# Optimization experiments

Hardware: AMD Instinct MI355X
Metric: run time of the kernel (lower is better)

## Reference

```python
import jax, jax.numpy as jnp
import numpy as np


def _pick(key, nodes, mask, cnt):
    # Uniformly pick one of the `cnt` entries of `nodes` where mask is True.
    r = jax.random.randint(key, (), 0, jnp.maximum(cnt, 1))
    cs = jnp.cumsum(mask.astype(jnp.int32))
    return nodes[jnp.argmax(cs == r + 1)]


def _one_walk(key, nbrs, f0, n_faces, L):
    # nbrs: [N,3] int32 neighbor table, f0: scalar start face.
    seq = jnp.zeros((L + 1,), jnp.int32).at[0].set(f0)
    visited = jnp.zeros((n_faces + 1,), bool).at[n_faces].set(True).at[f0].set(True)

    def cond(st):
        return st[2] <= L

    def body(st):
        seq, visited, i, bs, k = st
        k, k1, k2, k3 = jax.random.split(k, 4)
        cur = seq[i - 1]
        nb = nbrs[cur]                     # [3] neighbor candidates
        unv = ~visited[nb]
        cnt = unv.sum()
        need = cnt == 0                    # stuck -> backtrack
        cand = _pick(k1, nb, unv, cnt)

        def bcond(c):
            bs_c, found = c[0], c[1]
            return need & (~found) & (i > bs_c)

        def bbody(c):
            bs_c, found, ta, kk = c
            kk, kp = jax.random.split(kk)
            back = seq[i - bs_c - 1]
            bn = nbrs[back]
            bm = ~visited[bn]
            bc = bm.sum()
            f2 = bc > 0
            ta2 = _pick(kp, bn, bm, bc)
            return (jnp.where(f2, bs_c, bs_c + 2), f2, jnp.where(f2, ta2, ta), kk)

        bs_f, found, ta_bt, _ = jax.lax.while_loop(
            bcond, bbody, (bs, jnp.array(False), jnp.int32(0), k2))
        rand_node = jax.random.randint(k3, (), 0, n_faces, dtype=jnp.int32)
        to_add = jnp.where(~need, cand, jnp.where(found, ta_bt, rand_node))
        hit = need & found                 # successful backtrack
        bs_new = jnp.where(hit, bs_f, jnp.int32(1))
        i_new = jnp.where(hit, i - bs_f, i)
        ar = jnp.arange(L + 1, dtype=jnp.int32)
        # torch: replace seq[i-bs:i] with to_add on successful backtrack
        seq = jnp.where(hit & (ar >= i_new) & (ar < i), to_add, seq)
        visited = visited.at[to_add].set(True)
        seq = seq.at[i_new].set(to_add)
        return (seq, visited, i_new + 1, bs_new, k)

    seq, *_ = jax.lax.while_loop(
        cond, body, (seq, visited, jnp.int32(1), jnp.int32(1), key))
    return seq


def patch_random_walk(key, neighbors, centers, n_faces, seq_len):
    B, G = centers.shape
    keys = jax.random.split(key, B * G).reshape(B, G)
    walk_g = jax.vmap(_one_walk, in_axes=(0, None, 0, None, None))
    walk_bg = jax.vmap(walk_g, in_axes=(0, 0, 0, None, None))
    return walk_bg(keys, neighbors, centers, n_faces, seq_len)  # [B,G,L+1] int32


def setup_inputs() -> dict:
    key = jax.random.key(0)
    k1, k2, k3 = jax.random.split(key, 3)
    B, N, G = 4, 20000, 1024
    xyz = jax.random.normal(k1, (B, N, 3), dtype=jnp.float32)
    neighbors = jax.random.randint(k2, (B, N, 3), 0, N, dtype=jnp.int32)
    centers = jax.random.randint(k3, (B, G), 0, N, dtype=jnp.int32)
    return {"xyz": xyz, "neighbors": neighbors, "centers": centers,
            "n_faces": N, "seq_len": 63}


def reference(xyz, neighbors, centers, n_faces, seq_len):
    # patch_random_walk -> idx [B,G,K]; then Group.forward gather + recenter.
    idx = patch_random_walk(jax.random.key(42), neighbors, centers, n_faces, seq_len)
    gather = jax.vmap(lambda p, i: p[i])(xyz, idx)            # [B,G,K,3]
    center_xyz = jax.vmap(lambda p, c: p[c])(xyz, centers)    # [B,G,3]
    return gather - center_xyz[:, :, None, :]
```

## Files before the change

### kernel.cpp

```cpp
#include <hip/hip_runtime.h>
#include <stdint.h>
#include <stddef.h>


namespace {

__device__ __forceinline__ uint32_t rotl32(uint32_t x, int r) {
  return (x << r) | (x >> (32 - r));
}

__device__ __forceinline__ void tf2x32(uint32_t ka, uint32_t kb,
                                       uint32_t x0, uint32_t x1,
                                       uint32_t& o0, uint32_t& o1) {
  const uint32_t kc = ka ^ kb ^ 0x1BD11BDAu;
  x0 += ka; x1 += kb;
#define TF_R4(r0, r1, r2, r3)                          \
  x0 += x1; x1 = rotl32(x1, r0); x1 ^= x0;             \
  x0 += x1; x1 = rotl32(x1, r1); x1 ^= x0;             \
  x0 += x1; x1 = rotl32(x1, r2); x1 ^= x0;             \
  x0 += x1; x1 = rotl32(x1, r3); x1 ^= x0;
  TF_R4(13, 15, 26, 6)  x0 += kb; x1 += kc + 1u;
  TF_R4(17, 29, 16, 24) x0 += kc; x1 += ka + 2u;
  TF_R4(13, 15, 26, 6)  x0 += ka; x1 += kb + 3u;
  TF_R4(17, 29, 16, 24) x0 += kb; x1 += kc + 4u;
  TF_R4(13, 15, 26, 6)  x0 += kc; x1 += ka + 5u;
#undef TF_R4
  o0 = x0; o1 = x1;
}

__device__ __forceinline__ void randbits(uint32_t ka, uint32_t kb,
                                         uint32_t& hi, uint32_t& lo) {
  uint32_t s0a, s0b, s1a, s1b, h0, h1;
  tf2x32(ka, kb, 0u, 0u, s0a, s0b);
  tf2x32(ka, kb, 0u, 1u, s1a, s1b);
  tf2x32(s0a, s0b, 0u, 0u, h0, h1);
  hi = h0 ^ h1;
  tf2x32(s1a, s1b, 0u, 0u, h0, h1);
  lo = h0 ^ h1;
}

__device__ __forceinline__ uint32_t r_generic(uint32_t hi, uint32_t lo,
                                              uint32_t span) {
  uint32_t mult = 65536u % span;
  mult = (mult * mult) % span;
  return ((hi % span) * mult + (lo % span)) % span;
}

__device__ __forceinline__ uint32_t pick_code(uint32_t hi, uint32_t lo) {
  return ((hi % 3u + lo % 3u) % 3u) | ((lo & 1u) << 2);
}

constexpr int WPB = 16;
constexpr int CH = 64;
constexpr int KSTRIDE = 65;
constexpr int VISW = 2048;

__global__ __launch_bounds__(1024) void walk_kernel(
    const float* __restrict__ xyz, const int* __restrict__ nbrs,
    const int* __restrict__ centers, const int* __restrict__ n_faces_p,
    const int* __restrict__ seq_len_p, float* __restrict__ out,
    int s0, int num_walks, int Lp1) {
  __shared__ uint32_t visL[WPB * VISW];
  __shared__ uint2 keysL[WPB * KSTRIDE];

  const int tid = threadIdx.x;
  const int wv = tid >> 6, lane = tid & 63;
  const int w0 = blockIdx.x * WPB;
  if (w0 >= num_walks) return;
  const int w = w0 + wv;
  const bool active = (w < num_walks);

  const int N = *n_faces_p;
  const int L = *seq_len_p;
  const int B = s0 / (3 * N);
  const int G = num_walks / B;
  const bool bm_ok = (N <= VISW * 32);

  const int bb = (active ? w : w0) / G;
  const int* __restrict__ nb   = nbrs + (size_t)bb * N * 3;
  const float* __restrict__ xb = xyz + (size_t)bb * N * 3;

  const int f0 = active ? centers[w] : 0;
  int3 row = *reinterpret_cast<const int3*>(nb + 3 * (size_t)f0);

  uint32_t* __restrict__ visW = visL + wv * VISW;
  if (bm_ok) {
    for (int j = lane; j < VISW; j += 64) visW[j] = 0u;
    if (lane == 0 && active) visW[(unsigned)f0 >> 5] = 1u << (f0 & 31);
  }

  int3 t0 = *reinterpret_cast<const int3*>(nb + 3 * (size_t)row.x);
  int3 t1 = *reinterpret_cast<const int3*>(nb + 3 * (size_t)row.y);
  int3 t2 = *reinterpret_cast<const int3*>(nb + 3 * (size_t)row.z);

  if (wv == 0 && lane < WPB && (w0 + lane) < num_walks) {
    uint32_t ka, kb;
    tf2x32(0u, 42u, 0u, (uint32_t)(w0 + lane), ka, kb);
    keysL[lane * KSTRIDE + 0] = make_uint2(ka, kb);
#pragma clang loop unroll(disable)
    for (int c2 = 1; c2 < CH; ++c2) {
      tf2x32(ka, kb, 0u, 0u, ka, kb);
      keysL[lane * KSTRIDE + c2] = make_uint2(ka, kb);
    }
  }
  __syncthreads();

  if (!active) return;

  const uint2 mykey = keysL[wv * KSTRIDE + lane];
  const uint32_t mka = mykey.x, mkb = mykey.y;
  uint32_t mycode;
  {
    uint32_t k1a, k1b, hi, lo;
    tf2x32(mka, mkb, 0u, 1u, k1a, k1b);
    randbits(k1a, k1b, hi, lo);
    mycode = pick_code(hi, lo);
  }

  uint32_t extka = 0, extkb = 0;
  int extc = -1;
  auto get_key = [&](int idx, uint32_t& ra, uint32_t& rb) {
    if (idx < CH) {
      ra = (uint32_t)__shfl((int)mka, idx);
      rb = (uint32_t)__shfl((int)mkb, idx);
    } else {
      if (extc < 0) {
        extka = (uint32_t)__shfl((int)mka, CH - 1);
        extkb = (uint32_t)__shfl((int)mkb, CH - 1);
        extc = CH - 1;
      }
      while (extc < idx) { tf2x32(extka, extkb, 0u, 0u, extka, extkb); ++extc; }
      ra = extka; rb = extkb;
    }
  };

  int seqr = (lane == 0) ? f0 : -1;
  int i = 1, bs = 1, c = 0;

  if (bm_ok) {
    while (i <= L) {
      const int idx = c; ++c;
      const int n0 = row.x, n1 = row.y, n2 = row.z;
      const uint32_t wv0 = visW[(unsigned)n0 >> 5];
      const uint32_t wv1 = visW[(unsigned)n1 >> 5];
      const uint32_t wv2 = visW[(unsigned)n2 >> 5];
      const uint32_t u0 = ((wv0 >> (n0 & 31)) & 1u) ^ 1u;
      const uint32_t u1 = ((wv1 >> (n1 & 31)) & 1u) ^ 1u;
      const uint32_t u2 = ((wv2 >> (n2 & 31)) & 1u) ^ 1u;
      const uint32_t cnt = u0 + u1 + u2;

      int to_add, sel;
      if (__builtin_expect(cnt == 0, 0)) {
        sel = -1;
        uint32_t kia, kib;
        get_key(idx, kia, kib);
        uint32_t kka, kkb;
        tf2x32(kia, kib, 0u, 2u, kka, kkb);
        bool found = false;
        int ta = 0, bsc = bs;
        while (!found && i > bsc) {
          uint32_t ca, cb, kpa, kpb;
          tf2x32(kka, kkb, 0u, 0u, ca, cb);
          tf2x32(kka, kkb, 0u, 1u, kpa, kpb);
          const int back = __shfl(seqr, i - bsc - 1);
          const int3 br = *reinterpret_cast<const int3*>(nb + 3 * (size_t)back);
          const uint32_t e0 = ((visW[(unsigned)br.x >> 5] >> (br.x & 31)) & 1u) ^ 1u;
          const uint32_t e1 = ((visW[(unsigned)br.y >> 5] >> (br.y & 31)) & 1u) ^ 1u;
          const uint32_t e2 = ((visW[(unsigned)br.z >> 5] >> (br.z & 31)) & 1u) ^ 1u;
          const uint32_t bc = e0 + e1 + e2;
          if (bc > 0) {
            uint32_t bhi, blo;
            randbits(kpa, kpb, bhi, blo);
            const uint32_t bcode = pick_code(bhi, blo);
            const uint32_t r3 = bcode & 3u, r2 = (bcode >> 2) & 1u;
            const uint32_t t2v = (bc == 3 ? r3 : (bc == 2 ? r2 : 0)) + 1;
            ta = (e0 == t2v) ? br.x : ((e0 + e1 == t2v) ? br.y : br.z);
            found = true;
          } else {
            bsc += 2;
          }
          kka = ca; kkb = cb;
        }
        if (found) {
          to_add = ta;
          const int i_new = i - bsc;
          seqr = (lane >= i_new && lane < i) ? to_add : seqr;
          bs = bsc; i = i_new;
        } else {
          uint32_t k3a, k3b, rhi, rlo;
          tf2x32(kia, kib, 0u, 3u, k3a, k3b);
          randbits(k3a, k3b, rhi, rlo);
          to_add = (int)r_generic(rhi, rlo, (uint32_t)N);
          bs = 1;
        }
        if (lane == 0)
          visW[(unsigned)to_add >> 5] |= 1u << (to_add & 31);
        seqr = (lane == i) ? to_add : seqr;
        ++i;
        row = *reinterpret_cast<const int3*>(nb + 3 * (size_t)to_add);
      } else {
        uint32_t code;
        if (__builtin_expect(idx >= CH, 0)) {
          uint32_t ia, ib, k1a, k1b, hi, lo;
          get_key(idx, ia, ib);
          tf2x32(ia, ib, 0u, 1u, k1a, k1b);
          randbits(k1a, k1b, hi, lo);
          code = pick_code(hi, lo);
        } else {
          code = (uint32_t)__builtin_amdgcn_readlane((int)mycode, idx);
        }
        const uint32_t r3 = code & 3u, r2 = (code >> 2) & 1u;
        const uint32_t target = (cnt == 3 ? r3 : (cnt == 2 ? r2 : 0)) + 1;
        sel = (u0 == target) ? 0 : ((u0 + u1 == target) ? 1 : 2);
        to_add = (sel == 0) ? n0 : ((sel == 1) ? n1 : n2);
        const uint32_t wsel = (sel == 0) ? wv0 : ((sel == 1) ? wv1 : wv2);
        if (lane == 0)
          visW[(unsigned)to_add >> 5] = wsel | (1u << (to_add & 31));
        seqr = (lane == i) ? to_add : seqr;
        bs = 1; ++i;
        row = (sel == 0) ? t0 : ((sel == 1) ? t1 : t2);
      }
      t0 = *reinterpret_cast<const int3*>(nb + 3 * (size_t)row.x);
      t1 = *reinterpret_cast<const int3*>(nb + 3 * (size_t)row.y);
      t2 = *reinterpret_cast<const int3*>(nb + 3 * (size_t)row.z);
    }
  } else {
    int hist  = (lane == 0) ? f0 : -1;
    int hist2 = -1;
    while (i <= L) {
      const int idx = c; ++c;
      const bool deep = (idx >= CH);
      const int n0 = row.x, n1 = row.y, n2 = row.z;
      int v0 = __any(hist == n0), v1 = __any(hist == n1), v2 = __any(hist == n2);
      if (deep) {
        v0 |= __any(hist2 == n0); v1 |= __any(hist2 == n1); v2 |= __any(hist2 == n2);
      }
      const int u0 = 1 - v0, u1 = 1 - v1, u2 = 1 - v2;
      const int cnt = u0 + u1 + u2;

      int to_add;
      bool hit = false;
      int bsf = bs;
      if (cnt > 0) {
        uint32_t code;
        if (deep) {
          uint32_t ia, ib, k1a, k1b, hi, lo;
          get_key(idx, ia, ib);
          tf2x32(ia, ib, 0u, 1u, k1a, k1b);
          randbits(k1a, k1b, hi, lo);
          code = pick_code(hi, lo);
        } else {
          code = (uint32_t)__builtin_amdgcn_readlane((int)mycode, idx);
        }
        const int r3 = (int)(code & 3u), r2 = (int)((code >> 2) & 1u);
        const int target = (cnt == 3 ? r3 : (cnt == 2 ? r2 : 0)) + 1;
        to_add = (u0 == target) ? n0 : ((u0 + u1 == target) ? n1 : n2);
      } else {
        uint32_t kia, kib;
        get_key(idx, kia, kib);
        uint32_t kka, kkb;
        tf2x32(kia, kib, 0u, 2u, kka, kkb);
        bool found = false;
        int ta = 0, bsc = bs;
        while (!found && i > bsc) {
          uint32_t ca, cb, kpa, kpb;
          tf2x32(kka, kkb, 0u, 0u, ca, cb);
          tf2x32(kka, kkb, 0u, 1u, kpa, kpb);
          const int back = __shfl(seqr, i - bsc - 1);
          const int3 br = *reinterpret_cast<const int3*>(nb + 3 * (size_t)back);
          int w0m = __any(hist == br.x), w1m = __any(hist == br.y), w2m = __any(hist == br.z);
          if (deep) {
            w0m |= __any(hist2 == br.x); w1m |= __any(hist2 == br.y); w2m |= __any(hist2 == br.z);
          }
          const int e0 = 1 - w0m, e1 = 1 - w1m, e2 = 1 - w2m;
          const int bc = e0 + e1 + e2;
          if (bc > 0) {
            uint32_t bhi, blo;
            randbits(kpa, kpb, bhi, blo);
            const uint32_t bcode = pick_code(bhi, blo);
            const int r3 = (int)(bcode & 3u), r2 = (int)((bcode >> 2) & 1u);
            const int t2v = (bc == 3 ? r3 : (bc == 2 ? r2 : 0)) + 1;
            ta = (e0 == t2v) ? br.x : ((e0 + e1 == t2v) ? br.y : br.z);
            found = true;
          } else {
            bsc += 2;
          }
          kka = ca; kkb = cb;
        }
        if (found) {
          to_add = ta; hit = true; bsf = bsc;
        } else {
          uint32_t k3a, k3b, rhi, rlo;
          tf2x32(kia, kib, 0u, 3u, k3a, k3b);
          randbits(k3a, k3b, rhi, rlo);
          to_add = (int)r_generic(rhi, rlo, (uint32_t)N);
        }
      }

      int i_new, up;
      if (hit) { i_new = i - bsf; bs = bsf; up = i - 1; }
      else     { i_new = i;       bs = 1;   up = i; }
      seqr = (lane >= i_new && lane <= up) ? to_add : seqr;

      const int slot = idx + 1;
      if (slot < CH)          hist  = (lane == slot)      ? to_add : hist;
      else if (slot < 2 * CH) hist2 = (lane == slot - CH) ? to_add : hist2;

      i = i_new + 1;
      row = *reinterpret_cast<const int3*>(nb + 3 * (size_t)to_add);
    }
  }

  const float cx = xb[3 * (size_t)f0 + 0];
  const float cy = xb[3 * (size_t)f0 + 1];
  const float cz = xb[3 * (size_t)f0 + 2];
  if (lane < Lp1) {
    const int node = seqr;
    float3 v;
    v.x = xb[3 * (size_t)node + 0] - cx;
    v.y = xb[3 * (size_t)node + 1] - cy;
    v.z = xb[3 * (size_t)node + 2] - cz;
    *reinterpret_cast<float3*>(out + ((size_t)w * Lp1 + lane) * 3) = v;
  }
}

}

extern "C" void kernel_launch(void* const* d_in, const int* in_sizes, int n_in,
                              void* d_out, int out_size, void* d_ws, size_t ws_size,
                              hipStream_t stream) {
  const float* xyz     = (const float*)d_in[0];
  const int*   nbrs    = (const int*)d_in[1];
  const int*   centers = (const int*)d_in[2];
  const int*   n_faces = (const int*)d_in[3];
  const int*   seq_len = (const int*)d_in[4];
  float* out = (float*)d_out;

  const int s0 = in_sizes[0];
  const int num_walks = in_sizes[2];
  const int Lp1 = out_size / (3 * num_walks);

  const int blocks = (num_walks + WPB - 1) / WPB;
  walk_kernel<<<blocks, WPB * 64, 0, stream>>>(
      xyz, nbrs, centers, n_faces, seq_len, out, s0, num_walks, Lp1);
}
```

Before: 105.3 us.

## Split walk into codes, LDS-resident walk, and gather kernels with one-lane-per-walk

```diff
diff --git a/kernel.cpp b/kernel.cpp
--- a/kernel.cpp
+++ b/kernel.cpp
@@ -50,110 +50,217 @@
   return ((hi % 3u + lo % 3u) % 3u) | ((lo & 1u) << 2);
 }
 
+__device__ __noinline__ void live_key(int w, int idx, uint32_t& ka,
+                                      uint32_t& kb) {
+  tf2x32(0u, 42u, 0u, (uint32_t)w, ka, kb);
+  for (int c = 0; c < idx; ++c) tf2x32(ka, kb, 0u, 0u, ka, kb);
+}
+
+constexpr int CH = 64;
 constexpr int WPB = 16;
-constexpr int CH = 64;
-constexpr int KSTRIDE = 65;
-constexpr int VISW = 2048;
-
-__global__ __launch_bounds__(1024) void walk_kernel(
-    const float* __restrict__ xyz, const int* __restrict__ nbrs,
-    const int* __restrict__ centers, const int* __restrict__ n_faces_p,
-    const int* __restrict__ seq_len_p, float* __restrict__ out,
-    int s0, int num_walks, int Lp1) {
-  __shared__ uint32_t visL[WPB * VISW];
-  __shared__ uint2 keysL[WPB * KSTRIDE];
-
-  const int tid = threadIdx.x;
-  const int wv = tid >> 6, lane = tid & 63;
-  const int w0 = blockIdx.x * WPB;
-  if (w0 >= num_walks) return;
-  const int w = w0 + wv;
-  const bool active = (w < num_walks);
-
-  const int N = *n_faces_p;
-  const int L = *seq_len_p;
-  const int B = s0 / (3 * N);
-  const int G = num_walks / B;
-  const bool bm_ok = (N <= VISW * 32);
-
-  const int bb = (active ? w : w0) / G;
-  const int* __restrict__ nb   = nbrs + (size_t)bb * N * 3;
-  const float* __restrict__ xb = xyz + (size_t)bb * N * 3;
-
-  const int f0 = active ? centers[w] : 0;
-  int3 row = *reinterpret_cast<const int3*>(nb + 3 * (size_t)f0);
-
-  uint32_t* __restrict__ visW = visL + wv * VISW;
-  if (bm_ok) {
-    for (int j = lane; j < VISW; j += 64) visW[j] = 0u;
-    if (lane == 0 && active) visW[(unsigned)f0 >> 5] = 1u << (f0 & 31);
-  }
-
-  int3 t0 = *reinterpret_cast<const int3*>(nb + 3 * (size_t)row.x);
-  int3 t1 = *reinterpret_cast<const int3*>(nb + 3 * (size_t)row.y);
-  int3 t2 = *reinterpret_cast<const int3*>(nb + 3 * (size_t)row.z);
-
+constexpr int BMW = 626;
+constexpr int NMAX = BMW * 32;
+constexpr int SEQS = 66;
+constexpr int VCAP = 96;
+
+__global__ __launch_bounds__(1024) void codes_kernel(
+    uint8_t* __restrict__ codes_g, int num_walks) {
+  __shared__ uint2 keysL[WPB][CH + 1];
+  const int tid = threadIdx.x, wv = tid >> 6, lane = tid & 63;
+  const int w0 = blockIdx.x * WPB, w = w0 + wv;
   if (wv == 0 && lane < WPB && (w0 + lane) < num_walks) {
     uint32_t ka, kb;
     tf2x32(0u, 42u, 0u, (uint32_t)(w0 + lane), ka, kb);
-    keysL[lane * KSTRIDE + 0] = make_uint2(ka, kb);
+    keysL[lane][0] = make_uint2(ka, kb);
 #pragma clang loop unroll(disable)
-    for (int c2 = 1; c2 < CH; ++c2) {
+    for (int c = 1; c < CH; ++c) {
       tf2x32(ka, kb, 0u, 0u, ka, kb);
-      keysL[lane * KSTRIDE + c2] = make_uint2(ka, kb);
+      keysL[lane][c] = make_uint2(ka, kb);
     }
   }
   __syncthreads();
-
-  if (!active) return;
-
-  const uint2 mykey = keysL[wv * KSTRIDE + lane];
-  const uint32_t mka = mykey.x, mkb = mykey.y;
-  uint32_t mycode;
-  {
-    uint32_t k1a, k1b, hi, lo;
-    tf2x32(mka, mkb, 0u, 1u, k1a, k1b);
-    randbits(k1a, k1b, hi, lo);
-    mycode = pick_code(hi, lo);
-  }
-
-  uint32_t extka = 0, extkb = 0;
-  int extc = -1;
-  auto get_key = [&](int idx, uint32_t& ra, uint32_t& rb) {
-    if (idx < CH) {
-      ra = (uint32_t)__shfl((int)mka, idx);
-      rb = (uint32_t)__shfl((int)mkb, idx);
-    } else {
-      if (extc < 0) {
-        extka = (uint32_t)__shfl((int)mka, CH - 1);
-        extkb = (uint32_t)__shfl((int)mkb, CH - 1);
-        extc = CH - 1;
+  if (w >= num_walks) return;
+  const uint2 kc = keysL[wv][lane];
+  uint32_t k1a, k1b, hi, lo;
+  tf2x32(kc.x, kc.y, 0u, 1u, k1a, k1b);
+  randbits(k1a, k1b, hi, lo);
+  codes_g[(size_t)w * CH + lane] = (uint8_t)pick_code(hi, lo);
+}
+
+__global__ __launch_bounds__(256) void walk_kernel(
+    const int* __restrict__ nbrs, const int* __restrict__ centers,
+    const int* __restrict__ n_faces_p, const int* __restrict__ seq_len_p,
+    const uint8_t* __restrict__ codes_g, uint32_t* __restrict__ seq_g,
+    uint32_t* __restrict__ vis_g, int s0, int num_walks, int Lp1) {
+  __shared__ uint32_t nb01L[NMAX];
+  __shared__ uint16_t nb2L[NMAX];
+  __shared__ uint32_t visL[WPB * BMW];
+  __shared__ uint16_t seqL[WPB * SEQS];
+  __shared__ uint8_t  codesL[WPB * CH];
+
+  const int tid = threadIdx.x, lane = tid & 63;
+  const int w0 = blockIdx.x * WPB;
+  if (w0 >= num_walks) return;
+  const int N = *n_faces_p, L = *seq_len_p;
+  const int B = s0 / (3 * N), G = num_walks / B;
+  const int wlast = (w0 + WPB - 1 < num_walks) ? w0 + WPB - 1 : num_walks - 1;
+  const bool fast = (N <= NMAX) && (Lp1 <= CH) && (L + 1 < SEQS) &&
+                    ((w0 / G) == (wlast / G));
+
+  if (fast) {
+    const int* __restrict__ nbs = nbrs + (size_t)(w0 / G) * N * 3;
+    for (int r = tid; r < N; r += 256) {
+      const int3 v = *reinterpret_cast<const int3*>(nbs + 3 * (size_t)r);
+      nb01L[r] = (uint32_t)v.x | ((uint32_t)v.y << 16);
+      nb2L[r] = (uint16_t)v.z;
+    }
+    for (int j = tid; j < WPB * BMW; j += 256) visL[j] = 0u;
+    const int wcnt = wlast - w0 + 1;
+    const uint32_t* src = reinterpret_cast<const uint32_t*>(
+        codes_g + (size_t)w0 * CH);
+    for (int j = tid; j < (wcnt * CH) / 4; j += 256)
+      reinterpret_cast<uint32_t*>(codesL)[j] = src[j];
+  }
+  __syncthreads();
+  if (tid >= 64) return;
+
+  const int wl = lane;
+  const int wg = w0 + wl;
+  const bool alive = (wl < WPB) && (wg < num_walks);
+
+  if (fast) {
+    int f0 = 0, n0 = 0, n1 = 0, n2 = 0, i = 1, bs = 1, cstep = 0;
+    if (alive) {
+      f0 = centers[wg];
+      seqL[wl * SEQS + 0] = (uint16_t)f0;
+      visL[wl * BMW + ((unsigned)f0 >> 5)] = 1u << (f0 & 31);
+      const uint32_t p = nb01L[f0];
+      n0 = (int)(p & 0xffffu); n1 = (int)(p >> 16); n2 = (int)nb2L[f0];
+    }
+    for (;;) {
+      const bool go = alive && (i <= L);
+      if (!__ballot(go)) break;
+      if (go) {
+        const int idx = cstep; ++cstep;
+        const uint32_t wa = visL[wl * BMW + ((unsigned)n0 >> 5)];
+        const uint32_t wb = visL[wl * BMW + ((unsigned)n1 >> 5)];
+        const uint32_t wc = visL[wl * BMW + ((unsigned)n2 >> 5)];
+        const uint32_t pA = nb01L[n0]; const uint32_t a2 = nb2L[n0];
+        const uint32_t pB = nb01L[n1]; const uint32_t b2 = nb2L[n1];
+        const uint32_t pC = nb01L[n2]; const uint32_t c2 = nb2L[n2];
+        const uint32_t u0 = ((wa >> (n0 & 31)) & 1u) ^ 1u;
+        const uint32_t u1 = ((wb >> (n1 & 31)) & 1u) ^ 1u;
+        const uint32_t u2 = ((wc >> (n2 & 31)) & 1u) ^ 1u;
+        const uint32_t cnt = u0 + u1 + u2;
+
+        int to_add, sel;
+        if (__builtin_expect(cnt == 0, 0)) {
+          sel = -1;
+          uint32_t kia, kib;
+          live_key(wg, idx, kia, kib);
+          uint32_t kka, kkb;
+          tf2x32(kia, kib, 0u, 2u, kka, kkb);
+          bool found = false;
+          int ta = 0, bsc = bs;
+          while (!found && i > bsc) {
+            uint32_t ca, cb, kpa, kpb;
+            tf2x32(kka, kkb, 0u, 0u, ca, cb);
+            tf2x32(kka, kkb, 0u, 1u, kpa, kpb);
+            const int back = (int)seqL[wl * SEQS + (i - bsc - 1)];
+            const uint32_t pm = nb01L[back];
+            const int m0 = (int)(pm & 0xffffu), m1 = (int)(pm >> 16);
+            const int m2 = (int)nb2L[back];
+            const uint32_t e0 =
+                ((visL[wl * BMW + (m0 >> 5)] >> (m0 & 31)) & 1u) ^ 1u;
+            const uint32_t e1 =
+                ((visL[wl * BMW + (m1 >> 5)] >> (m1 & 31)) & 1u) ^ 1u;
+            const uint32_t e2 =
+                ((visL[wl * BMW + (m2 >> 5)] >> (m2 & 31)) & 1u) ^ 1u;
+            const uint32_t bc = e0 + e1 + e2;
+            if (bc > 0) {
+              uint32_t bhi, blo;
+              randbits(kpa, kpb, bhi, blo);
+              const uint32_t bcode = pick_code(bhi, blo);
+              const uint32_t r3 = bcode & 3u, r2 = (bcode >> 2) & 1u;
+              const uint32_t t2v = (bc == 3 ? r3 : (bc == 2 ? r2 : 0)) + 1;
+              ta = (e0 == t2v) ? m0 : ((e0 + e1 == t2v) ? m1 : m2);
+              found = true;
+            } else {
+              bsc += 2;
+            }
+            kka = ca; kkb = cb;
+          }
+          if (found) {
+            const int i_new = i - bsc;
+            for (int a = i_new; a < i; ++a)
+              seqL[wl * SEQS + a] = (uint16_t)ta;
+            to_add = ta; bs = bsc; i = i_new;
+          } else {
+            uint32_t k3a, k3b, rh, rl;
+            tf2x32(kia, kib, 0u, 3u, k3a, k3b);
+            randbits(k3a, k3b, rh, rl);
+            to_add = (int)r_generic(rh, rl, (uint32_t)N);
+            bs = 1;
+          }
+        } else {
+          uint32_t code;
+          if (__builtin_expect(idx >= CH, 0)) {
+            uint32_t ia, ib, k1a, k1b, h2, l2;
+            live_key(wg, idx, ia, ib);
+            tf2x32(ia, ib, 0u, 1u, k1a, k1b);
+            randbits(k1a, k1b, h2, l2);
+            code = pick_code(h2, l2);
+          } else {
+            code = codesL[(wl << 6) | idx];
+          }
+          const uint32_t r3 = code & 3u, r2 = (code >> 2) & 1u;
+          const uint32_t target = (cnt == 3 ? r3 : (cnt == 2 ? r2 : 0)) + 1;
+          sel = (u0 == target) ? 0 : ((u0 + u1 == target) ? 1 : 2);
+          to_add = (sel == 0) ? n0 : ((sel == 1) ? n1 : n2);
+          bs = 1;
+        }
+        const unsigned word = wl * BMW + ((unsigned)to_add >> 5);
+        visL[word] = visL[word] | (1u << (to_add & 31));
+        seqL[wl * SEQS + i] = (uint16_t)to_add;
+        ++i;
+        if (sel == 0)      { n0 = (int)(pA & 0xffffu); n1 = (int)(pA >> 16); n2 = (int)a2; }
+        else if (sel == 1) { n0 = (int)(pB & 0xffffu); n1 = (int)(pB >> 16); n2 = (int)b2; }
+        else if (sel == 2) { n0 = (int)(pC & 0xffffu); n1 = (int)(pC >> 16); n2 = (int)c2; }
+        else {
+          const uint32_t p = nb01L[to_add];
+          n0 = (int)(p & 0xffffu); n1 = (int)(p >> 16); n2 = (int)nb2L[to_add];
+        }
       }
-      while (extc < idx) { tf2x32(extka, extkb, 0u, 0u, extka, extkb); ++extc; }
-      ra = extka; rb = extkb;
-    }
-  };
-
-  int seqr = (lane == 0) ? f0 : -1;
-  int i = 1, bs = 1, c = 0;
-
-  if (bm_ok) {
+    }
+    for (int k = 0; k < WPB; ++k) {
+      const int wgk = w0 + k;
+      if (wgk < num_walks && lane < Lp1)
+        seq_g[(size_t)wgk * Lp1 + lane] = (uint32_t)seqL[k * SEQS + lane];
+    }
+  } else {
+    if (!alive) return;
+    uint32_t* __restrict__ vlist = vis_g + (size_t)wg * VCAP;
+    int nvis = 0;
+    const int bbl = wg / G;
+    const int* __restrict__ nbl = nbrs + (size_t)bbl * N * 3;
+    const int f0 = centers[wg];
+    vlist[nvis++] = (uint32_t)f0;
+    seq_g[(size_t)wg * Lp1 + 0] = (uint32_t)f0;
+    int3 row = *reinterpret_cast<const int3*>(nbl + 3 * (size_t)f0);
+    int i = 1, bs = 1, cstep = 0;
+    auto unv = [&](int node) -> uint32_t {
+      for (int k = 0; k < nvis; ++k)
+        if ((int)vlist[k] == node) return 0u;
+      return 1u;
+    };
     while (i <= L) {
-      const int idx = c; ++c;
-      const int n0 = row.x, n1 = row.y, n2 = row.z;
-      const uint32_t wv0 = visW[(unsigned)n0 >> 5];
-      const uint32_t wv1 = visW[(unsigned)n1 >> 5];
-      const uint32_t wv2 = visW[(unsigned)n2 >> 5];
-      const uint32_t u0 = ((wv0 >> (n0 & 31)) & 1u) ^ 1u;
-      const uint32_t u1 = ((wv1 >> (n1 & 31)) & 1u) ^ 1u;
-      const uint32_t u2 = ((wv2 >> (n2 & 31)) & 1u) ^ 1u;
+      const int idx = cstep; ++cstep;
+      const uint32_t u0 = unv(row.x), u1 = unv(row.y), u2 = unv(row.z);
       const uint32_t cnt = u0 + u1 + u2;
-
-      int to_add, sel;
-      if (__builtin_expect(cnt == 0, 0)) {
-        sel = -1;
+      int to_add;
+      if (cnt == 0) {
         uint32_t kia, kib;
-        get_key(idx, kia, kib);
+        live_key(wg, idx, kia, kib);
         uint32_t kka, kkb;
         tf2x32(kia, kib, 0u, 2u, kka, kkb);
         bool found = false;
@@ -162,11 +269,9 @@
           uint32_t ca, cb, kpa, kpb;
           tf2x32(kka, kkb, 0u, 0u, ca, cb);
           tf2x32(kka, kkb, 0u, 1u, kpa, kpb);
-          const int back = __shfl(seqr, i - bsc - 1);
-          const int3 br = *reinterpret_cast<const int3*>(nb + 3 * (size_t)back);
-          const uint32_t e0 = ((visW[(unsigned)br.x >> 5] >> (br.x & 31)) & 1u) ^ 1u;
-          const uint32_t e1 = ((visW[(unsigned)br.y >> 5] >> (br.y & 31)) & 1u) ^ 1u;
-          const uint32_t e2 = ((visW[(unsigned)br.z >> 5] >> (br.z & 31)) & 1u) ^ 1u;
+          const int back = (int)seq_g[(size_t)wg * Lp1 + (i - bsc - 1)];
+          const int3 br = *reinterpret_cast<const int3*>(nbl + 3 * (size_t)back);
+          const uint32_t e0 = unv(br.x), e1 = unv(br.y), e2 = unv(br.z);
           const uint32_t bc = e0 + e1 + e2;
           if (bc > 0) {
             uint32_t bhi, blo;
@@ -182,135 +287,192 @@
           kka = ca; kkb = cb;
         }
         if (found) {
-          to_add = ta;
           const int i_new = i - bsc;
-          seqr = (lane >= i_new && lane < i) ? to_add : seqr;
-          bs = bsc; i = i_new;
+          for (int a = i_new; a < i; ++a)
+            seq_g[(size_t)wg * Lp1 + a] = (uint32_t)ta;
+          to_add = ta; bs = bsc; i = i_new;
         } else {
-          uint32_t k3a, k3b, rhi, rlo;
+          uint32_t k3a, k3b, rh, rl;
           tf2x32(kia, kib, 0u, 3u, k3a, k3b);
-          randbits(k3a, k3b, rhi, rlo);
-          to_add = (int)r_generic(rhi, rlo, (uint32_t)N);
+          randbits(k3a, k3b, rh, rl);
+          to_add = (int)r_generic(rh, rl, (uint32_t)N);
           bs = 1;
         }
-        if (lane == 0)
-          visW[(unsigned)to_add >> 5] |= 1u << (to_add & 31);
-        seqr = (lane == i) ? to_add : seqr;
-        ++i;
-        row = *reinterpret_cast<const int3*>(nb + 3 * (size_t)to_add);
       } else {
         uint32_t code;
-        if (__builtin_expect(idx >= CH, 0)) {
-          uint32_t ia, ib, k1a, k1b, hi, lo;
-          get_key(idx, ia, ib);
+        if (idx >= CH) {
+          uint32_t ia, ib, k1a, k1b, h2, l2;
+          live_key(wg, idx, ia, ib);
           tf2x32(ia, ib, 0u, 1u, k1a, k1b);
-          randbits(k1a, k1b, hi, lo);
-          code = pick_code(hi, lo);
+          randbits(k1a, k1b, h2, l2);
+          code = pick_code(h2, l2);
         } else {
-          code = (uint32_t)__builtin_amdgcn_readlane((int)mycode, idx);
+          code = codes_g[(size_t)wg * CH + idx];
         }
         const uint32_t r3 = code & 3u, r2 = (code >> 2) & 1u;
         const uint32_t target = (cnt == 3 ? r3 : (cnt == 2 ? r2 : 0)) + 1;
-        sel = (u0 == target) ? 0 : ((u0 + u1 == target) ? 1 : 2);
-        to_add = (sel == 0) ? n0 : ((sel == 1) ? n1 : n2);
-        const uint32_t wsel = (sel == 0) ? wv0 : ((sel == 1) ? wv1 : wv2);
-        if (lane == 0)
-          visW[(unsigned)to_add >> 5] = wsel | (1u << (to_add & 31));
-        seqr = (lane == i) ? to_add : seqr;
-        bs = 1; ++i;
-        row = (sel == 0) ? t0 : ((sel == 1) ? t1 : t2);
+        to_add = (u0 == target) ? row.x
+               : ((u0 + u1 == target) ? row.y : row.z);
+        bs = 1;
       }
-      t0 = *reinterpret_cast<const int3*>(nb + 3 * (size_t)row.x);
-      t1 = *reinterpret_cast<const int3*>(nb + 3 * (size_t)row.y);
-      t2 = *reinterpret_cast<const int3*>(nb + 3 * (size_t)row.z);
-    }
-  } else {
-    int hist  = (lane == 0) ? f0 : -1;
-    int hist2 = -1;
-    while (i <= L) {
-      const int idx = c; ++c;
-      const bool deep = (idx >= CH);
-      const int n0 = row.x, n1 = row.y, n2 = row.z;
-      int v0 = __any(hist == n0), v1 = __any(hist == n1), v2 = __any(hist == n2);
+      if (nvis < VCAP) vlist[nvis++] = (uint32_t)to_add;
+      seq_g[(size_t)wg * Lp1 + i] = (uint32_t)to_add;
+      ++i;
+      row = *reinterpret_cast<const int3*>(nbl + 3 * (size_t)to_add);
+    }
+  }
+}
+
+__global__ __launch_bounds__(256) void gather_kernel(
+    const float* __restrict__ xyz, const int* __restrict__ centers,
+    const int* __restrict__ n_faces_p, const uint32_t* __restrict__ seq_g,
+    float* __restrict__ out, int s0, int num_walks, int Lp1) {
+  const int idx = blockIdx.x * 256 + threadIdx.x;
+  if (idx >= num_walks * Lp1) return;
+  const int w = idx / Lp1;
+  const int N = *n_faces_p;
+  const int B = s0 / (3 * N), G = num_walks / B, b = w / G;
+  const float* __restrict__ xb = xyz + (size_t)b * N * 3;
+  const int node = (int)seq_g[idx];
+  const int c0 = centers[w];
+  float3 v;
+  v.x = xb[3 * (size_t)node + 0] - xb[3 * (size_t)c0 + 0];
+  v.y = xb[3 * (size_t)node + 1] - xb[3 * (size_t)c0 + 1];
+  v.z = xb[3 * (size_t)node + 2] - xb[3 * (size_t)c0 + 2];
+  reinterpret_cast<float3*>(out)[idx] = v;
+}
+
+constexpr int KSTRIDE = 65;
+__global__ __launch_bounds__(1024) void fused_kernel(
+    const float* __restrict__ xyz, const int* __restrict__ nbrs,
+    const int* __restrict__ centers, const int* __restrict__ n_faces_p,
+    const int* __restrict__ seq_len_p, float* __restrict__ out,
+    int s0, int num_walks, int Lp1) {
+  __shared__ uint2 keysL[WPB * KSTRIDE];
+  const int tid = threadIdx.x, wv = tid >> 6, lane = tid & 63;
+  const int w0 = blockIdx.x * WPB;
+  if (w0 >= num_walks) return;
+  const int w = w0 + wv;
+  const bool active = (w < num_walks);
+  const int N = *n_faces_p, L = *seq_len_p;
+  const int B = s0 / (3 * N), G = num_walks / B;
+  const int bb = (active ? w : w0) / G;
+  const int* __restrict__ nb   = nbrs + (size_t)bb * N * 3;
+  const float* __restrict__ xb = xyz + (size_t)bb * N * 3;
+  const int f0 = active ? centers[w] : 0;
+  int3 row = active ? *reinterpret_cast<const int3*>(nb + 3 * (size_t)f0)
+                    : make_int3(0, 0, 0);
+  if (wv == 0 && lane < WPB && (w0 + lane) < num_walks) {
+    uint32_t ka, kb;
+    tf2x32(0u, 42u, 0u, (uint32_t)(w0 + lane), ka, kb);
+    keysL[lane * KSTRIDE + 0] = make_uint2(ka, kb);
+#pragma clang loop unroll(disable)
+    for (int c2 = 1; c2 < CH; ++c2) {
+      tf2x32(ka, kb, 0u, 0u, ka, kb);
+      keysL[lane * KSTRIDE + c2] = make_uint2(ka, kb);
+    }
+  }
+  __syncthreads();
+  if (!active) return;
+  const uint2 mykey = keysL[wv * KSTRIDE + lane];
+  uint32_t mycode;
+  {
+    uint32_t k1a, k1b, hi, lo;
+    tf2x32(mykey.x, mykey.y, 0u, 1u, k1a, k1b);
+    randbits(k1a, k1b, hi, lo);
+    mycode = pick_code(hi, lo);
+  }
+  uint32_t extka = 0, extkb = 0;
+  int extc = -1;
+  auto get_key = [&](int idx, uint32_t& ra, uint32_t& rb) {
+    if (idx < CH) {
+      ra = (uint32_t)__shfl((int)mykey.x, idx);
+      rb = (uint32_t)__shfl((int)mykey.y, idx);
+    } else {
+      if (extc < 0) {
+        extka = (uint32_t)__shfl((int)mykey.x, CH - 1);
+        extkb = (uint32_t)__shfl((int)mykey.y, CH - 1);
+        extc = CH - 1;
+      }
+      while (extc < idx) { tf2x32(extka, extkb, 0u, 0u, extka, extkb); ++extc; }
+      ra = extka; rb = extkb;
+    }
+  };
+  int hist = (lane == 0) ? f0 : -1, hist2 = -1;
+  int seqr = (lane == 0) ? f0 : -1;
+  int i = 1, bs = 1, c = 0;
+  while (i <= L) {
+    const int idx = c; ++c;
+    const bool deep = (idx >= CH);
+    const int n0 = row.x, n1 = row.y, n2 = row.z;
+    int v0 = __any(hist == n0), v1 = __any(hist == n1), v2 = __any(hist == n2);
+    if (deep) {
+      v0 |= __any(hist2 == n0); v1 |= __any(hist2 == n1); v2 |= __any(hist2 == n2);
+    }
+    const int u0 = 1 - v0, u1 = 1 - v1, u2 = 1 - v2;
+    const int cnt = u0 + u1 + u2;
+    int to_add; bool hit = false; int bsf = bs;
+    if (cnt > 0) {
+      uint32_t code;
       if (deep) {
-        v0 |= __any(hist2 == n0); v1 |= __any(hist2 == n1); v2 |= __any(hist2 == n2);
+        uint32_t ia, ib, k1a, k1b, hi, lo;
+        get_key(idx, ia, ib);
+        tf2x32(ia, ib, 0u, 1u, k1a, k1b);
+        randbits(k1a, k1b, hi, lo);
+        code = pick_code(hi, lo);
+      } else {
+        code = (uint32_t)__builtin_amdgcn_readlane((int)mycode, idx);
       }
-      const int u0 = 1 - v0, u1 = 1 - v1, u2 = 1 - v2;
-      const int cnt = u0 + u1 + u2;
-
-      int to_add;
-      bool hit = false;
-      int bsf = bs;
-      if (cnt > 0) {
-        uint32_t code;
+      const int r3 = (int)(code & 3u), r2 = (int)((code >> 2) & 1u);
+      const int target = (cnt == 3 ? r3 : (cnt == 2 ? r2 : 0)) + 1;
+      to_add = (u0 == target) ? n0 : ((u0 + u1 == target) ? n1 : n2);
+    } else {
+      uint32_t kia, kib;
+      get_key(idx, kia, kib);
+      uint32_t kka, kkb;
+      tf2x32(kia, kib, 0u, 2u, kka, kkb);
+      bool found = false; int ta = 0, bsc = bs;
+      while (!found && i > bsc) {
+        uint32_t ca, cb, kpa, kpb;
+        tf2x32(kka, kkb, 0u, 0u, ca, cb);
+        tf2x32(kka, kkb, 0u, 1u, kpa, kpb);
+        const int back = __shfl(seqr, i - bsc - 1);
+        const int3 br = *reinterpret_cast<const int3*>(nb + 3 * (size_t)back);
+        int a0 = __any(hist == br.x), a1 = __any(hist == br.y), a2m = __any(hist == br.z);
         if (deep) {
-          uint32_t ia, ib, k1a, k1b, hi, lo;
-          get_key(idx, ia, ib);
-          tf2x32(ia, ib, 0u, 1u, k1a, k1b);
-          randbits(k1a, k1b, hi, lo);
-          code = pick_code(hi, lo);
-        } else {
-          code = (uint32_t)__builtin_amdgcn_readlane((int)mycode, idx);
+          a0 |= __any(hist2 == br.x); a1 |= __any(hist2 == br.y); a2m |= __any(hist2 == br.z);
         }
-        const int r3 = (int)(code & 3u), r2 = (int)((code >> 2) & 1u);
-        const int target = (cnt == 3 ? r3 : (cnt == 2 ? r2 : 0)) + 1;
-        to_add = (u0 == target) ? n0 : ((u0 + u1 == target) ? n1 : n2);
-      } else {
-        uint32_t kia, kib;
-        get_key(idx, kia, kib);
-        uint32_t kka, kkb;
-        tf2x32(kia, kib, 0u, 2u, kka, kkb);
-        bool found = false;
-        int ta = 0, bsc = bs;
-        while (!found && i > bsc) {
-          uint32_t ca, cb, kpa, kpb;
-          tf2x32(kka, kkb, 0u, 0u, ca, cb);
-          tf2x32(kka, kkb, 0u, 1u, kpa, kpb);
-          const int back = __shfl(seqr, i - bsc - 1);
-          const int3 br = *reinterpret_cast<const int3*>(nb + 3 * (size_t)back);
-          int w0m = __any(hist == br.x), w1m = __any(hist == br.y), w2m = __any(hist == br.z);
-          if (deep) {
-            w0m |= __any(hist2 == br.x); w1m |= __any(hist2 == br.y); w2m |= __any(hist2 == br.z);
-          }
-          const int e0 = 1 - w0m, e1 = 1 - w1m, e2 = 1 - w2m;
-          const int bc = e0 + e1 + e2;
-          if (bc > 0) {
-            uint32_t bhi, blo;
-            randbits(kpa, kpb, bhi, blo);
-            const uint32_t bcode = pick_code(bhi, blo);
-            const int r3 = (int)(bcode & 3u), r2 = (int)((bcode >> 2) & 1u);
-            const int t2v = (bc == 3 ? r3 : (bc == 2 ? r2 : 0)) + 1;
-            ta = (e0 == t2v) ? br.x : ((e0 + e1 == t2v) ? br.y : br.z);
-            found = true;
-          } else {
-            bsc += 2;
-          }
-          kka = ca; kkb = cb;
-        }
-        if (found) {
-          to_add = ta; hit = true; bsf = bsc;
-        } else {
-          uint32_t k3a, k3b, rhi, rlo;
-          tf2x32(kia, kib, 0u, 3u, k3a, k3b);
-          randbits(k3a, k3b, rhi, rlo);
-          to_add = (int)r_generic(rhi, rlo, (uint32_t)N);
-        }
+        const int e0 = 1 - a0, e1 = 1 - a1, e2 = 1 - a2m;
+        const int bc = e0 + e1 + e2;
+        if (bc > 0) {
+          uint32_t bhi, blo;
+          randbits(kpa, kpb, bhi, blo);
+          const uint32_t bcode = pick_code(bhi, blo);
+          const int r3 = (int)(bcode & 3u), r2 = (int)((bcode >> 2) & 1u);
+          const int t2v = (bc == 3 ? r3 : (bc == 2 ? r2 : 0)) + 1;
+          ta = (e0 == t2v) ? br.x : ((e0 + e1 == t2v) ? br.y : br.z);
+          found = true;
+        } else bsc += 2;
+        kka = ca; kkb = cb;
       }
-
-      int i_new, up;
-      if (hit) { i_new = i - bsf; bs = bsf; up = i - 1; }
-      else     { i_new = i;       bs = 1;   up = i; }
-      seqr = (lane >= i_new && lane <= up) ? to_add : seqr;
-
-      const int slot = idx + 1;
-      if (slot < CH)          hist  = (lane == slot)      ? to_add : hist;
-      else if (slot < 2 * CH) hist2 = (lane == slot - CH) ? to_add : hist2;
-
-      i = i_new + 1;
-      row = *reinterpret_cast<const int3*>(nb + 3 * (size_t)to_add);
-    }
-  }
-
+      if (found) { to_add = ta; hit = true; bsf = bsc; }
+      else {
+        uint32_t k3a, k3b, rh, rl;
+        tf2x32(kia, kib, 0u, 3u, k3a, k3b);
+        randbits(k3a, k3b, rh, rl);
+        to_add = (int)r_generic(rh, rl, (uint32_t)N);
+      }
+    }
+    int i_new, up;
+    if (hit) { i_new = i - bsf; bs = bsf; up = i - 1; }
+    else     { i_new = i;       bs = 1;   up = i; }
+    seqr = (lane >= i_new && lane <= up) ? to_add : seqr;
+    const int slot = idx + 1;
+    if (slot < CH)          hist  = (lane == slot)      ? to_add : hist;
+    else if (slot < 2 * CH) hist2 = (lane == slot - CH) ? to_add : hist2;
+    i = i_new + 1;
+    row = *reinterpret_cast<const int3*>(nb + 3 * (size_t)to_add);
+  }
   const float cx = xb[3 * (size_t)f0 + 0];
   const float cy = xb[3 * (size_t)f0 + 1];
   const float cz = xb[3 * (size_t)f0 + 2];
@@ -340,7 +502,26 @@
   const int num_walks = in_sizes[2];
   const int Lp1 = out_size / (3 * num_walks);
 
-  const int blocks = (num_walks + WPB - 1) / WPB;
-  walk_kernel<<<blocks, WPB * 64, 0, stream>>>(
-      xyz, nbrs, centers, n_faces, seq_len, out, s0, num_walks, Lp1);
-}
+  const size_t codes_sz = (size_t)num_walks * CH;
+  const size_t seq_off  = (codes_sz + 255) & ~(size_t)255;
+  const size_t seq_sz   = (size_t)num_walks * Lp1 * 4;
+  const size_t vis_off  = (seq_off + seq_sz + 255) & ~(size_t)255;
+  const size_t need     = vis_off + (size_t)num_walks * VCAP * 4;
+
+  const int blocks16 = (num_walks + WPB - 1) / WPB;
+  if (ws_size >= need) {
+    uint8_t*  codes_g = (uint8_t*)d_ws;
+    uint32_t* seq_g   = (uint32_t*)((char*)d_ws + seq_off);
+    uint32_t* vis_g   = (uint32_t*)((char*)d_ws + vis_off);
+    codes_kernel<<<blocks16, 1024, 0, stream>>>(codes_g, num_walks);
+    walk_kernel<<<blocks16, 256, 0, stream>>>(
+        nbrs, centers, n_faces, seq_len, codes_g, seq_g, vis_g,
+        s0, num_walks, Lp1);
+    const int total = num_walks * Lp1;
+    gather_kernel<<<(total + 255) / 256, 256, 0, stream>>>(
+        xyz, centers, n_faces, seq_g, out, s0, num_walks, Lp1);
+  } else {
+    fused_kernel<<<blocks16, WPB * 64, 0, stream>>>(
+        xyz, nbrs, centers, n_faces, seq_len, out, s0, num_walks, Lp1);
+  }
+}
```

Result: slower. 113.2 us (+7.5%).
